# Optimization experiments

Measured on AMD Instinct MI355X. Metric: run time of the kernel, lower is better.

## Reference

```python
import jax, jax.numpy as jnp
import numpy as np

B, S, D, H = 4, 1024, 1024, 16
HD = D // H  # 64
NEG = -10000000.0


def setup_inputs() -> dict:
    key = jax.random.key(0)
    ks = jax.random.split(key, 8)
    x = jax.random.normal(ks[0], (B, S, D), dtype=jnp.float32)
    adj = jax.random.randint(ks[1], (B, S, S), 0, 2).astype(jnp.float32)
    scale = 1.0 / np.sqrt(D)
    Wq = jax.random.normal(ks[2], (D, D), dtype=jnp.float32) * scale
    bq = jnp.zeros((D,), dtype=jnp.float32)
    Wk = jax.random.normal(ks[3], (D, D), dtype=jnp.float32) * scale
    bk = jnp.zeros((D,), dtype=jnp.float32)
    Wv = jax.random.normal(ks[4], (D, D), dtype=jnp.float32) * scale
    bv = jnp.zeros((D,), dtype=jnp.float32)
    return {"x": x, "adj": adj, "Wq": Wq, "bq": bq, "Wk": Wk, "bk": bk, "Wv": Wv, "bv": bv}


def reference(x, adj, Wq, bq, Wk, bk, Wv, bv):
    # QKV projections, split into heads: [B,S,D] -> [B,H,S,HD]
    def heads(t):
        return t.reshape(B, S, H, HD).transpose(0, 2, 1, 3)

    q = heads(x @ Wq + bq)
    k = heads(x @ Wk + bk)
    v = heads(x @ Wv + bv)

    # scaled scores [B,H,S,S]
    scores = jnp.einsum('bhqd,bhkd->bhqk', q, k) / jnp.sqrt(jnp.asarray(HD, x.dtype))
    # adjacency mask: 0 where adj>=0.5 else -1e7, broadcast over heads
    mask_add = jnp.where(adj < 0.5, jnp.asarray(NEG, x.dtype), jnp.asarray(0.0, x.dtype))
    scores = scores + mask_add[:, None, :, :]

    probs = jax.nn.softmax(scores, axis=-1)
    ctx = jnp.einsum('bhqk,bhkd->bhqd', probs, v)  # [B,H,S,HD]
    ctx = ctx.transpose(0, 2, 1, 3).reshape(B, S, D)
    h = jax.nn.relu(ctx)
    return (h, adj)
```

## Files before the change

kernel.cpp:

```cpp
#include <hip/hip_runtime.h>

constexpr int Bn  = 4;
constexpr int Sn  = 1024;
constexpr int Dn  = 1024;
constexpr int Hn  = 16;
constexpr int HDn = 64;

using short8   = __attribute__((ext_vector_type(8))) short;
using float4v  = __attribute__((ext_vector_type(4))) float;
using float16v = __attribute__((ext_vector_type(16))) float;

__device__ __forceinline__ ushort f2bf(float f) {
    union { float f; unsigned u; } v; v.f = f;
    unsigned r = v.u + 0x7fff + ((v.u >> 16) & 1);
    return (ushort)(r >> 16);
}

__device__ __forceinline__ void gload16(const void* g, void* l) {
    __builtin_amdgcn_global_load_lds(
        (const __attribute__((address_space(1))) void*)g,
        (__attribute__((address_space(3))) void*)l, 16, 0, 0);
}

__global__ __launch_bounds__(256) void prep(
    const float* __restrict__ x,
    const float* __restrict__ Wq, const float* __restrict__ Wk,
    const float* __restrict__ Wv, const float* __restrict__ adj,
    ushort* __restrict__ xb, ushort* __restrict__ Wt, uint* __restrict__ Mb)
{
    const int bx  = blockIdx.x;
    const int tid = threadIdx.x;
    __shared__ __align__(16) ushort T[64 * 72];

    if (bx < 2048) {
        const size_t i = ((size_t)bx * 256 + tid) * 8;
        float4 a = *(const float4*)&x[i];
        float4 b = *(const float4*)&x[i + 4];
        ushort o[8] = {f2bf(a.x), f2bf(a.y), f2bf(a.z), f2bf(a.w),
                       f2bf(b.x), f2bf(b.y), f2bf(b.z), f2bf(b.w)};
        *(uint4*)&xb[i] = *(const uint4*)o;
    } else if (bx < 2816) {
        const int idx = bx - 2048;
        const int which = idx >> 8, rem = idx & 255;
        const float* __restrict__ W = (which == 0) ? Wq : (which == 1) ? Wk : Wv;
        ushort* __restrict__ O = Wt + (size_t)which * Dn * Dn;
        const int k0 = (rem & 15) * 64, n0 = (rem >> 4) * 64;

        const int kl = tid >> 4, nl = (tid & 15) * 4;
#pragma unroll
        for (int p = 0; p < 4; ++p) {
            float4 w4 = *(const float4*)&W[(size_t)(k0 + p * 16 + kl) * Dn + n0 + nl];
            T[(nl + 0) * 72 + p * 16 + kl] = f2bf(w4.x);
            T[(nl + 1) * 72 + p * 16 + kl] = f2bf(w4.y);
            T[(nl + 2) * 72 + p * 16 + kl] = f2bf(w4.z);
            T[(nl + 3) * 72 + p * 16 + kl] = f2bf(w4.w);
        }
        __syncthreads();
        const int nr = tid >> 2, kc = (tid & 3) * 16;
        uint4 u0 = *(const uint4*)&T[nr * 72 + kc];
        uint4 u1 = *(const uint4*)&T[nr * 72 + kc + 8];
        *(uint4*)&O[(size_t)(n0 + nr) * Dn + k0 + kc]     = u0;
        *(uint4*)&O[(size_t)(n0 + nr) * Dn + k0 + kc + 8] = u1;
    } else {
        const int rid  = (bx - 2816) * 256 + tid;
        const int lane = rid & 63;
        const int w    = (rid >> 6) & 3;
        const int kt   = (rid >> 8) & 15;
        const int qt   = (rid >> 12) & 7;
        const int b    = rid >> 15;
        const int col  = lane & 31, hi = lane >> 5;
        const int q    = qt * 128 + w * 32 + col;
        const float* arow = adj + ((size_t)b * Sn + q) * Sn + kt * 64;

        uint words[16];
#pragma unroll
        for (int mt = 0; mt < 2; ++mt)
#pragma unroll
            for (int pr = 0; pr < 8; ++pr) {
                const int r0 = 2 * pr;
                const int k0l = mt * 32 + (r0 & 3) + 8 * (r0 >> 2) + 4 * hi;
                float2 a = *(const float2*)&arow[k0l];
                words[mt * 8 + pr] = (a.x >= 0.5f ? 0x0000FFFFu : 0u) |
                                     (a.y >= 0.5f ? 0xFFFF0000u : 0u);
            }
        uint* dst = Mb + (size_t)rid * 16;
#pragma unroll
        for (int c = 0; c < 4; ++c)
            *(uint4*)&dst[c * 4] = make_uint4(words[c*4], words[c*4+1], words[c*4+2], words[c*4+3]);
    }
}

__global__ __launch_bounds__(256) void qkv_gemm(
    const ushort* __restrict__ xb, const ushort* __restrict__ Wt,
    const float* __restrict__ bq, const float* __restrict__ bk,
    const float* __restrict__ bv,
    ushort* __restrict__ Qb, ushort* __restrict__ Kb, ushort* __restrict__ Vb)
{
    const int which = blockIdx.z;
    const ushort* __restrict__ Bw   = Wt + (size_t)which * Dn * Dn;
    const float* __restrict__  bias = (which == 0) ? bq : (which == 1) ? bk : bv;
    ushort* __restrict__       Out  = (which == 0) ? Qb : (which == 1) ? Kb : Vb;
    const float scale = (which == 0) ? 0.18033688011112042f : 1.0f;

    const int n0   = blockIdx.x * 128;
    const int m0   = blockIdx.y * 128;
    const int tid  = threadIdx.x;
    const int wave = tid >> 6;
    const int lane = tid & 63;
    const int wm   = wave >> 1;
    const int wn   = wave & 1;

    __shared__ __align__(16) ushort As[128 * 32];
    __shared__ __align__(16) ushort Bs[128 * 32];

    const int L0 = wave * 64 + lane;
    const int r0s = L0 >> 2, c0s = (L0 & 3) * 8;
    const int L1 = L0 + 256;
    const int r1s = L1 >> 2, c1s = (L1 & 3) * 8;

    const ushort* pA0 = &xb[(size_t)(m0 + r0s) * Dn + c0s];
    const ushort* pA1 = &xb[(size_t)(m0 + r1s) * Dn + c1s];
    const ushort* pB0 = &Bw[(size_t)(n0 + r0s) * Dn + c0s];
    const ushort* pB1 = &Bw[(size_t)(n0 + r1s) * Dn + c1s];

    char* ldsA0 = (char*)As + wave * 1024;
    char* ldsA1 = (char*)As + wave * 1024 + 4096;
    char* ldsB0 = (char*)Bs + wave * 1024;
    char* ldsB1 = (char*)Bs + wave * 1024 + 4096;

    const int mlane = lane & 15;
    const int kg    = (lane >> 4) * 8;

    float4v acc[4][4];
    const float4v z4 = {0.f, 0.f, 0.f, 0.f};
#pragma unroll
    for (int i = 0; i < 4; ++i)
#pragma unroll
        for (int j = 0; j < 4; ++j) acc[i][j] = z4;

    for (int k0 = 0; k0 < Dn; k0 += 32) {
        __syncthreads();
        gload16(pA0, ldsA0);
        gload16(pA1, ldsA1);
        gload16(pB0, ldsB0);
        gload16(pB1, ldsB1);
        pA0 += 32; pA1 += 32; pB0 += 32; pB1 += 32;
        __syncthreads();

        short8 af[4], bf[4];
#pragma unroll
        for (int i = 0; i < 4; ++i)
            af[i] = *(const short8*)&As[(wm * 64 + i * 16 + mlane) * 32 + kg];
#pragma unroll
        for (int j = 0; j < 4; ++j)
            bf[j] = *(const short8*)&Bs[(wn * 64 + j * 16 + mlane) * 32 + kg];
#pragma unroll
        for (int i = 0; i < 4; ++i)
#pragma unroll
            for (int j = 0; j < 4; ++j)
                acc[i][j] = __builtin_amdgcn_mfma_f32_16x16x32_bf16(af[i], bf[j], acc[i][j], 0, 0, 0);
    }

    const int rb  = (lane >> 4) * 4;
    const int col = lane & 15;
#pragma unroll
    for (int j = 0; j < 4; ++j) {
        const int n  = n0 + wn * 64 + j * 16 + col;
        const float bias_n = bias[n];
        const int h  = n >> 6;
        const int hd = n & 63;
#pragma unroll
        for (int i = 0; i < 4; ++i) {
#pragma unroll
            for (int r = 0; r < 4; ++r) {
                const int m = m0 + wm * 64 + i * 16 + rb + r;
                const int b = m >> 10;
                const int s = m & 1023;
                size_t addr;
                if (which == 2)
                    addr = (((size_t)(b * Hn + h)) * HDn + hd) * Sn + s;
                else
                    addr = (((size_t)(b * Hn + h)) * Sn + s) * HDn + hd;
                Out[addr] = f2bf((acc[i][j][r] + bias_n) * scale);
            }
        }
    }
}

__global__ __launch_bounds__(256, 2) void attn_mfma(
    const ushort* __restrict__ Q, const ushort* __restrict__ K,
    const ushort* __restrict__ Vt, const uint* __restrict__ Mw,
    float* __restrict__ out)
{
    const int qt = blockIdx.x, h = blockIdx.y, b = blockIdx.z;
    const int tid  = threadIdx.x;
    const int w    = tid >> 6, lane = tid & 63;
    const int col  = lane & 31, hi = lane >> 5;

    const size_t hb = ((size_t)(b * Hn + h)) * Sn * HDn;
    const ushort* Kg = K + hb;
    const ushort* Vg = Vt + hb;

    __shared__ __align__(16) ushort Ks[2][64 * 72];
    __shared__ __align__(16) ushort Vs[2][64 * 72];

    short8 qf[4];
#pragma unroll
    for (int kp = 0; kp < 4; ++kp)
        qf[kp] = *(const short8*)&Q[hb +
            (size_t)(qt * 128 + w * 32 + col) * HDn + kp * 16 + hi * 8];

    float16v o_[2];
#pragma unroll
    for (int dt = 0; dt < 2; ++dt)
#pragma unroll
        for (int r = 0; r < 16; ++r) o_[dt][r] = 0.f;
    float ls = 0.f;

    const int c0 = tid, c1 = tid + 256;
    const int la0 = (c0 >> 3) * 72 + (c0 & 7) * 8;
    const int la1 = (c1 >> 3) * 72 + (c1 & 7) * 8;

    uint4 k0 = *(const uint4*)&Kg[(size_t)(c0 >> 3) * HDn + (c0 & 7) * 8];
    uint4 k1 = *(const uint4*)&Kg[(size_t)(c1 >> 3) * HDn + (c1 & 7) * 8];
    uint4 v0 = *(const uint4*)&Vg[(size_t)(c0 >> 3) * Sn + (c0 & 7) * 8];
    uint4 v1 = *(const uint4*)&Vg[(size_t)(c1 >> 3) * Sn + (c1 & 7) * 8];
    *(uint4*)&Ks[0][la0] = k0;  *(uint4*)&Ks[0][la1] = k1;
    *(uint4*)&Vs[0][la0] = v0;  *(uint4*)&Vs[0][la1] = v1;
    __syncthreads();

    const uint* mbase = Mw + ((size_t)((b * 8 + qt) * 16) * 4 + w) * 1024 + lane * 16;

    for (int kt = 0; kt < 16; ++kt) {
        const int cur = kt & 1;
        if (kt < 15) {
            k0 = *(const uint4*)&Kg[(size_t)((kt + 1) * 64 + (c0 >> 3)) * HDn + (c0 & 7) * 8];
            k1 = *(const uint4*)&Kg[(size_t)((kt + 1) * 64 + (c1 >> 3)) * HDn + (c1 & 7) * 8];
            v0 = *(const uint4*)&Vg[(size_t)(c0 >> 3) * Sn + (kt + 1) * 64 + (c0 & 7) * 8];
            v1 = *(const uint4*)&Vg[(size_t)(c1 >> 3) * Sn + (kt + 1) * 64 + (c1 & 7) * 8];
        }
        const uint* mp = mbase + (size_t)kt * 4096;
        uint4 mk4[4];
        mk4[0] = *(const uint4*)(mp);
        mk4[1] = *(const uint4*)(mp + 4);
        mk4[2] = *(const uint4*)(mp + 8);
        mk4[3] = *(const uint4*)(mp + 12);
        const uint* mka = (const uint*)mk4;

#pragma unroll
        for (int mt = 0; mt < 2; ++mt) {
            float16v s_;
#pragma unroll
            for (int r = 0; r < 16; ++r) s_[r] = 0.f;
#pragma unroll
            for (int kp = 0; kp < 4; ++kp) {
                short8 ak = *(const short8*)&Ks[cur][(mt * 32 + col) * 72 + kp * 16 + hi * 8];
                s_ = __builtin_amdgcn_mfma_f32_32x32x16_bf16(ak, qf[kp], s_, 0, 0, 0);
            }

            unsigned up[8];
#pragma unroll
            for (int pr = 0; pr < 8; ++pr) {
                const unsigned e0 = __float_as_uint(exp2f(s_[2 * pr]))     + 0x8000u;
                const unsigned e1 = __float_as_uint(exp2f(s_[2 * pr + 1])) + 0x8000u;
                const unsigned u  = __builtin_amdgcn_perm(e1, e0, 0x07060302u) & mka[mt * 8 + pr];
                up[pr] = u;
                ls += __uint_as_float(u << 16) + __uint_as_float(u & 0xffff0000u);
            }

#pragma unroll
            for (int kh = 0; kh < 2; ++kh) {
                const unsigned a0 = up[kh * 4 + 0], a1 = up[kh * 4 + 1];
                const unsigned a2 = up[kh * 4 + 2], a3 = up[kh * 4 + 3];
                const unsigned t0 = (unsigned)__shfl_xor((int)(hi ? a0 : a2), 32, 64);
                const unsigned t1 = (unsigned)__shfl_xor((int)(hi ? a1 : a3), 32, 64);
                union { short8 s; unsigned u[4]; } f;
                f.u[0] = hi ? t0 : a0;
                f.u[1] = hi ? t1 : a1;
                f.u[2] = hi ? a2 : t0;
                f.u[3] = hi ? a3 : t1;
                const int kp = mt * 2 + kh;
#pragma unroll
                for (int dt = 0; dt < 2; ++dt) {
                    short8 av = *(const short8*)&Vs[cur][(dt * 32 + col) * 72 + kp * 16 + hi * 8];
                    o_[dt] = __builtin_amdgcn_mfma_f32_32x32x16_bf16(av, f.s, o_[dt], 0, 0, 0);
                }
            }
        }

        if (kt < 15) {
            const int nxt = cur ^ 1;
            *(uint4*)&Ks[nxt][la0] = k0;  *(uint4*)&Ks[nxt][la1] = k1;
            *(uint4*)&Vs[nxt][la0] = v0;  *(uint4*)&Vs[nxt][la1] = v1;
        }
        __syncthreads();
    }

    float l = ls + (float)__shfl_xor((float)ls, 32, 64);
    const float inv = 1.0f / l;
    const int q = qt * 128 + w * 32 + col;
    float* op = &out[((size_t)b * Sn + q) * Dn + h * 64];
#pragma unroll
    for (int dt = 0; dt < 2; ++dt)
#pragma unroll
        for (int rg = 0; rg < 4; ++rg) {
            const int d = dt * 32 + rg * 8 + hi * 4;
            float4 o4;
            o4.x = fmaxf(o_[dt][rg * 4 + 0] * inv, 0.0f);
            o4.y = fmaxf(o_[dt][rg * 4 + 1] * inv, 0.0f);
            o4.z = fmaxf(o_[dt][rg * 4 + 2] * inv, 0.0f);
            o4.w = fmaxf(o_[dt][rg * 4 + 3] * inv, 0.0f);
            *(float4*)&op[d] = o4;
        }
}

extern "C" void kernel_launch(void* const* d_in, const int* in_sizes, int n_in,
                              void* d_out, int out_size, void* d_ws, size_t ws_size,
                              hipStream_t stream)
{
    const float* x   = (const float*)d_in[0];
    const float* adj = (const float*)d_in[1];
    const float* Wq  = (const float*)d_in[2];
    const float* bq  = (const float*)d_in[3];
    const float* Wk  = (const float*)d_in[4];
    const float* bk  = (const float*)d_in[5];
    const float* Wv  = (const float*)d_in[6];
    const float* bv  = (const float*)d_in[7];
    float* out = (float*)d_out;

    ushort* xb = (ushort*)d_ws;
    ushort* Wt = xb + (size_t)Bn * Sn * Dn;
    ushort* Qb = Wt + (size_t)3 * Dn * Dn;
    ushort* Kb = Qb + (size_t)Bn * Hn * Sn * HDn;
    ushort* Vb = Kb + (size_t)Bn * Hn * Sn * HDn;
    uint*   Mb = (uint*)(Vb + (size_t)Bn * Hn * Sn * HDn);

    prep<<<dim3(3328), 256, 0, stream>>>(x, Wq, Wk, Wv, adj, xb, Wt, Mb);

    qkv_gemm<<<dim3(Dn / 128, (Bn * Sn) / 128, 3), 256, 0, stream>>>(
        xb, Wt, bq, bk, bv, Qb, Kb, Vb);

    attn_mfma<<<dim3(8, Hn, Bn), 256, 0, stream>>>(Qb, Kb, Vb, Mb, out);

    hipMemcpyAsync(out + (size_t)Bn * Sn * Dn, adj,
                   (size_t)Bn * Sn * Sn * sizeof(float),
                   hipMemcpyDeviceToDevice, stream);
}
```

Baseline: 191.0 us.

## Split attention key range across waves with LDS reduction; split prep kernel

The attention kernel now gives each block 32 queries and has its four waves each handle a quarter of the key range. K and V are read straight from global memory instead of being staged in double-buffered LDS, and the partial outputs and row sums are combined through an LDS reduction at the end. The grid grows fourfold and launch bounds rise to 4 blocks per CU, trading more K/V global traffic for more parallelism and occupancy. The prep kernel is also split into three separate launches, which adds launch overhead.

```diff
diff --git a/kernel.cpp b/kernel.cpp
--- a/kernel.cpp
+++ b/kernel.cpp
@@ -22,72 +22,78 @@
         (__attribute__((address_space(3))) void*)l, 16, 0, 0);
 }
 
-__global__ __launch_bounds__(256) void prep(
-    const float* __restrict__ x,
+__global__ __launch_bounds__(256) void convert_x(const float* __restrict__ x,
+                                                 ushort* __restrict__ xb)
+{
+    const size_t i = ((size_t)blockIdx.x * 256 + threadIdx.x) * 8;
+    float4 a = *(const float4*)&x[i];
+    float4 b = *(const float4*)&x[i + 4];
+    ushort o[8] = {f2bf(a.x), f2bf(a.y), f2bf(a.z), f2bf(a.w),
+                   f2bf(b.x), f2bf(b.y), f2bf(b.z), f2bf(b.w)};
+    *(uint4*)&xb[i] = *(const uint4*)o;
+}
+
+__global__ __launch_bounds__(256) void transpose_w(
     const float* __restrict__ Wq, const float* __restrict__ Wk,
-    const float* __restrict__ Wv, const float* __restrict__ adj,
-    ushort* __restrict__ xb, ushort* __restrict__ Wt, uint* __restrict__ Mb)
-{
-    const int bx  = blockIdx.x;
-    const int tid = threadIdx.x;
+    const float* __restrict__ Wv, ushort* __restrict__ Wt)
+{
+    const int which = blockIdx.z;
+    const float* __restrict__ W = (which == 0) ? Wq : (which == 1) ? Wk : Wv;
+    ushort* __restrict__ O = Wt + (size_t)which * Dn * Dn;
+
+    const int k0 = blockIdx.x * 64;
+    const int n0 = blockIdx.y * 64;
+    const int t  = threadIdx.x;
+
     __shared__ __align__(16) ushort T[64 * 72];
 
-    if (bx < 2048) {
-        const size_t i = ((size_t)bx * 256 + tid) * 8;
-        float4 a = *(const float4*)&x[i];
-        float4 b = *(const float4*)&x[i + 4];
-        ushort o[8] = {f2bf(a.x), f2bf(a.y), f2bf(a.z), f2bf(a.w),
-                       f2bf(b.x), f2bf(b.y), f2bf(b.z), f2bf(b.w)};
-        *(uint4*)&xb[i] = *(const uint4*)o;
-    } else if (bx < 2816) {
-        const int idx = bx - 2048;
-        const int which = idx >> 8, rem = idx & 255;
-        const float* __restrict__ W = (which == 0) ? Wq : (which == 1) ? Wk : Wv;
-        ushort* __restrict__ O = Wt + (size_t)which * Dn * Dn;
-        const int k0 = (rem & 15) * 64, n0 = (rem >> 4) * 64;
-
-        const int kl = tid >> 4, nl = (tid & 15) * 4;
-#pragma unroll
-        for (int p = 0; p < 4; ++p) {
-            float4 w4 = *(const float4*)&W[(size_t)(k0 + p * 16 + kl) * Dn + n0 + nl];
-            T[(nl + 0) * 72 + p * 16 + kl] = f2bf(w4.x);
-            T[(nl + 1) * 72 + p * 16 + kl] = f2bf(w4.y);
-            T[(nl + 2) * 72 + p * 16 + kl] = f2bf(w4.z);
-            T[(nl + 3) * 72 + p * 16 + kl] = f2bf(w4.w);
+    const int kl = t >> 4;
+    const int nl = (t & 15) * 4;
+#pragma unroll
+    for (int p = 0; p < 4; ++p) {
+        float4 w = *(const float4*)&W[(size_t)(k0 + p * 16 + kl) * Dn + n0 + nl];
+        T[(nl + 0) * 72 + p * 16 + kl] = f2bf(w.x);
+        T[(nl + 1) * 72 + p * 16 + kl] = f2bf(w.y);
+        T[(nl + 2) * 72 + p * 16 + kl] = f2bf(w.z);
+        T[(nl + 3) * 72 + p * 16 + kl] = f2bf(w.w);
+    }
+    __syncthreads();
+    const int nr = t >> 2;
+    const int kc = (t & 3) * 16;
+    uint4 u0 = *(const uint4*)&T[nr * 72 + kc];
+    uint4 u1 = *(const uint4*)&T[nr * 72 + kc + 8];
+    *(uint4*)&O[(size_t)(n0 + nr) * Dn + k0 + kc]     = u0;
+    *(uint4*)&O[(size_t)(n0 + nr) * Dn + k0 + kc + 8] = u1;
+}
+
+__global__ __launch_bounds__(256) void build_mask(const float* __restrict__ adj,
+                                                  uint* __restrict__ Mb)
+{
+    const int rid  = blockIdx.x * 256 + threadIdx.x;
+    const int lane = rid & 63;
+    const int w    = (rid >> 6) & 3;
+    const int kt   = (rid >> 8) & 15;
+    const int qt   = (rid >> 12) & 7;
+    const int b    = rid >> 15;
+    const int col  = lane & 31, hi = lane >> 5;
+    const int q    = qt * 128 + w * 32 + col;
+    const float* arow = adj + ((size_t)b * Sn + q) * Sn + kt * 64;
+
+    uint words[16];
+#pragma unroll
+    for (int mt = 0; mt < 2; ++mt)
+#pragma unroll
+        for (int pr = 0; pr < 8; ++pr) {
+            const int r0 = 2 * pr;
+            const int k0l = mt * 32 + (r0 & 3) + 8 * (r0 >> 2) + 4 * hi;
+            float2 a = *(const float2*)&arow[k0l];
+            words[mt * 8 + pr] = (a.x >= 0.5f ? 0x0000FFFFu : 0u) |
+                                 (a.y >= 0.5f ? 0xFFFF0000u : 0u);
         }
-        __syncthreads();
-        const int nr = tid >> 2, kc = (tid & 3) * 16;
-        uint4 u0 = *(const uint4*)&T[nr * 72 + kc];
-        uint4 u1 = *(const uint4*)&T[nr * 72 + kc + 8];
-        *(uint4*)&O[(size_t)(n0 + nr) * Dn + k0 + kc]     = u0;
-        *(uint4*)&O[(size_t)(n0 + nr) * Dn + k0 + kc + 8] = u1;
-    } else {
-        const int rid  = (bx - 2816) * 256 + tid;
-        const int lane = rid & 63;
-        const int w    = (rid >> 6) & 3;
-        const int kt   = (rid >> 8) & 15;
-        const int qt   = (rid >> 12) & 7;
-        const int b    = rid >> 15;
-        const int col  = lane & 31, hi = lane >> 5;
-        const int q    = qt * 128 + w * 32 + col;
-        const float* arow = adj + ((size_t)b * Sn + q) * Sn + kt * 64;
-
-        uint words[16];
-#pragma unroll
-        for (int mt = 0; mt < 2; ++mt)
-#pragma unroll
-            for (int pr = 0; pr < 8; ++pr) {
-                const int r0 = 2 * pr;
-                const int k0l = mt * 32 + (r0 & 3) + 8 * (r0 >> 2) + 4 * hi;
-                float2 a = *(const float2*)&arow[k0l];
-                words[mt * 8 + pr] = (a.x >= 0.5f ? 0x0000FFFFu : 0u) |
-                                     (a.y >= 0.5f ? 0xFFFF0000u : 0u);
-            }
-        uint* dst = Mb + (size_t)rid * 16;
-#pragma unroll
-        for (int c = 0; c < 4; ++c)
-            *(uint4*)&dst[c * 4] = make_uint4(words[c*4], words[c*4+1], words[c*4+2], words[c*4+3]);
-    }
+    uint* dst = Mb + (size_t)rid * 16;
+#pragma unroll
+    for (int c = 0; c < 4; ++c)
+        *(uint4*)&dst[c * 4] = make_uint4(words[c*4], words[c*4+1], words[c*4+2], words[c*4+3]);
 }
 
 __global__ __launch_bounds__(256) void qkv_gemm(
@@ -187,12 +193,12 @@
     }
 }
 
-__global__ __launch_bounds__(256, 2) void attn_mfma(
+__global__ __launch_bounds__(256, 4) void attn_mfma(
     const ushort* __restrict__ Q, const ushort* __restrict__ K,
     const ushort* __restrict__ Vt, const uint* __restrict__ Mw,
     float* __restrict__ out)
 {
-    const int qt = blockIdx.x, h = blockIdx.y, b = blockIdx.z;
+    const int qsub = blockIdx.x, h = blockIdx.y, b = blockIdx.z;
     const int tid  = threadIdx.x;
     const int w    = tid >> 6, lane = tid & 63;
     const int col  = lane & 31, hi = lane >> 5;
@@ -201,14 +207,12 @@
     const ushort* Kg = K + hb;
     const ushort* Vg = Vt + hb;
 
-    __shared__ __align__(16) ushort Ks[2][64 * 72];
-    __shared__ __align__(16) ushort Vs[2][64 * 72];
+    __shared__ __align__(16) float red[3 * 64 * 34];
 
     short8 qf[4];
 #pragma unroll
     for (int kp = 0; kp < 4; ++kp)
-        qf[kp] = *(const short8*)&Q[hb +
-            (size_t)(qt * 128 + w * 32 + col) * HDn + kp * 16 + hi * 8];
+        qf[kp] = *(const short8*)&Q[hb + (size_t)(qsub * 32 + col) * HDn + kp * 16 + hi * 8];
 
     float16v o_[2];
 #pragma unroll
@@ -217,61 +221,43 @@
         for (int r = 0; r < 16; ++r) o_[dt][r] = 0.f;
     float ls = 0.f;
 
-    const int c0 = tid, c1 = tid + 256;
-    const int la0 = (c0 >> 3) * 72 + (c0 & 7) * 8;
-    const int la1 = (c1 >> 3) * 72 + (c1 & 7) * 8;
-
-    uint4 k0 = *(const uint4*)&Kg[(size_t)(c0 >> 3) * HDn + (c0 & 7) * 8];
-    uint4 k1 = *(const uint4*)&Kg[(size_t)(c1 >> 3) * HDn + (c1 & 7) * 8];
-    uint4 v0 = *(const uint4*)&Vg[(size_t)(c0 >> 3) * Sn + (c0 & 7) * 8];
-    uint4 v1 = *(const uint4*)&Vg[(size_t)(c1 >> 3) * Sn + (c1 & 7) * 8];
-    *(uint4*)&Ks[0][la0] = k0;  *(uint4*)&Ks[0][la1] = k1;
-    *(uint4*)&Vs[0][la0] = v0;  *(uint4*)&Vs[0][la1] = v1;
-    __syncthreads();
-
-    const uint* mbase = Mw + ((size_t)((b * 8 + qt) * 16) * 4 + w) * 1024 + lane * 16;
-
-    for (int kt = 0; kt < 16; ++kt) {
-        const int cur = kt & 1;
-        if (kt < 15) {
-            k0 = *(const uint4*)&Kg[(size_t)((kt + 1) * 64 + (c0 >> 3)) * HDn + (c0 & 7) * 8];
-            k1 = *(const uint4*)&Kg[(size_t)((kt + 1) * 64 + (c1 >> 3)) * HDn + (c1 & 7) * 8];
-            v0 = *(const uint4*)&Vg[(size_t)(c0 >> 3) * Sn + (kt + 1) * 64 + (c0 & 7) * 8];
-            v1 = *(const uint4*)&Vg[(size_t)(c1 >> 3) * Sn + (kt + 1) * 64 + (c1 & 7) * 8];
-        }
-        const uint* mp = mbase + (size_t)kt * 4096;
-        uint4 mk4[4];
-        mk4[0] = *(const uint4*)(mp);
-        mk4[1] = *(const uint4*)(mp + 4);
-        mk4[2] = *(const uint4*)(mp + 8);
-        mk4[3] = *(const uint4*)(mp + 12);
-        const uint* mka = (const uint*)mk4;
+    const int qt = qsub >> 2, wq = qsub & 3;
+    const uint* mb0 = Mw + ((size_t)((b * 8 + qt) * 16) * 4 + wq) * 1024 + lane * 16;
+
+#pragma unroll
+    for (int kk = 0; kk < 4; ++kk) {
+        const int kt = w * 4 + kk;
+        const uint* mp = mb0 + (size_t)kt * 4096;
 
 #pragma unroll
         for (int mt = 0; mt < 2; ++mt) {
             float16v s_;
 #pragma unroll
             for (int r = 0; r < 16; ++r) s_[r] = 0.f;
+            const ushort* krow = &Kg[(size_t)(kt * 64 + mt * 32 + col) * HDn + hi * 8];
 #pragma unroll
             for (int kp = 0; kp < 4; ++kp) {
-                short8 ak = *(const short8*)&Ks[cur][(mt * 32 + col) * 72 + kp * 16 + hi * 8];
+                short8 ak = *(const short8*)&krow[kp * 16];
                 s_ = __builtin_amdgcn_mfma_f32_32x32x16_bf16(ak, qf[kp], s_, 0, 0, 0);
             }
 
+            uint4 mA = *(const uint4*)(mp + mt * 8);
+            uint4 mB = *(const uint4*)(mp + mt * 8 + 4);
+            const uint mka[8] = {mA.x, mA.y, mA.z, mA.w, mB.x, mB.y, mB.z, mB.w};
             unsigned up[8];
 #pragma unroll
             for (int pr = 0; pr < 8; ++pr) {
                 const unsigned e0 = __float_as_uint(exp2f(s_[2 * pr]))     + 0x8000u;
                 const unsigned e1 = __float_as_uint(exp2f(s_[2 * pr + 1])) + 0x8000u;
-                const unsigned u  = __builtin_amdgcn_perm(e1, e0, 0x07060302u) & mka[mt * 8 + pr];
+                const unsigned u  = __builtin_amdgcn_perm(e1, e0, 0x07060302u) & mka[pr];
                 up[pr] = u;
                 ls += __uint_as_float(u << 16) + __uint_as_float(u & 0xffff0000u);
             }
 
 #pragma unroll
-            for (int kh = 0; kh < 2; ++kh) {
-                const unsigned a0 = up[kh * 4 + 0], a1 = up[kh * 4 + 1];
-                const unsigned a2 = up[kh * 4 + 2], a3 = up[kh * 4 + 3];
+            for (int kkh = 0; kkh < 2; ++kkh) {
+                const unsigned a0 = up[kkh * 4 + 0], a1 = up[kkh * 4 + 1];
+                const unsigned a2 = up[kkh * 4 + 2], a3 = up[kkh * 4 + 3];
                 const unsigned t0 = (unsigned)__shfl_xor((int)(hi ? a0 : a2), 32, 64);
                 const unsigned t1 = (unsigned)__shfl_xor((int)(hi ? a1 : a3), 32, 64);
                 union { short8 s; unsigned u[4]; } f;
@@ -279,39 +265,57 @@
                 f.u[1] = hi ? t1 : a1;
                 f.u[2] = hi ? a2 : t0;
                 f.u[3] = hi ? a3 : t1;
-                const int kp = mt * 2 + kh;
+                const int kp = mt * 2 + kkh;
 #pragma unroll
                 for (int dt = 0; dt < 2; ++dt) {
-                    short8 av = *(const short8*)&Vs[cur][(dt * 32 + col) * 72 + kp * 16 + hi * 8];
+                    short8 av = *(const short8*)&Vg[(size_t)(dt * 32 + col) * Sn
+                                                    + kt * 64 + kp * 16 + hi * 8];
                     o_[dt] = __builtin_amdgcn_mfma_f32_32x32x16_bf16(av, f.s, o_[dt], 0, 0, 0);
                 }
             }
         }
-
-        if (kt < 15) {
-            const int nxt = cur ^ 1;
-            *(uint4*)&Ks[nxt][la0] = k0;  *(uint4*)&Ks[nxt][la1] = k1;
-            *(uint4*)&Vs[nxt][la0] = v0;  *(uint4*)&Vs[nxt][la1] = v1;
+    }
+
+    if (w > 0) {
+        float* p = red + (size_t)((w - 1) * 64 + lane) * 34;
+#pragma unroll
+        for (int dt = 0; dt < 2; ++dt)
+#pragma unroll
+            for (int c = 0; c < 4; ++c)
+                *(float4*)&p[dt * 16 + c * 4] = make_float4(
+                    o_[dt][c * 4 + 0], o_[dt][c * 4 + 1],
+                    o_[dt][c * 4 + 2], o_[dt][c * 4 + 3]);
+        p[32] = ls;
+    }
+    __syncthreads();
+    if (w == 0) {
+#pragma unroll
+        for (int ww = 0; ww < 3; ++ww) {
+            const float* p = red + (size_t)(ww * 64 + lane) * 34;
+#pragma unroll
+            for (int dt = 0; dt < 2; ++dt)
+#pragma unroll
+                for (int r = 0; r < 16; ++r) o_[dt][r] += p[dt * 16 + r];
+            ls += p[32];
         }
-        __syncthreads();
-    }
-
-    float l = ls + (float)__shfl_xor((float)ls, 32, 64);
-    const float inv = 1.0f / l;
-    const int q = qt * 128 + w * 32 + col;
-    float* op = &out[((size_t)b * Sn + q) * Dn + h * 64];
-#pragma unroll
-    for (int dt = 0; dt < 2; ++dt)
-#pragma unroll
-        for (int rg = 0; rg < 4; ++rg) {
-            const int d = dt * 32 + rg * 8 + hi * 4;
-            float4 o4;
-            o4.x = fmaxf(o_[dt][rg * 4 + 0] * inv, 0.0f);
-            o4.y = fmaxf(o_[dt][rg * 4 + 1] * inv, 0.0f);
-            o4.z = fmaxf(o_[dt][rg * 4 + 2] * inv, 0.0f);
-            o4.w = fmaxf(o_[dt][rg * 4 + 3] * inv, 0.0f);
-            *(float4*)&op[d] = o4;
-        }
+
+        float l = ls + (float)__shfl_xor((float)ls, 32, 64);
+        const float inv = 1.0f / l;
+        const int q = qsub * 32 + col;
+        float* op = &out[((size_t)b * Sn + q) * Dn + h * 64];
+#pragma unroll
+        for (int dt = 0; dt < 2; ++dt)
+#pragma unroll
+            for (int rg = 0; rg < 4; ++rg) {
+                const int d = dt * 32 + rg * 8 + hi * 4;
+                float4 o4;
+                o4.x = fmaxf(o_[dt][rg * 4 + 0] * inv, 0.0f);
+                o4.y = fmaxf(o_[dt][rg * 4 + 1] * inv, 0.0f);
+                o4.z = fmaxf(o_[dt][rg * 4 + 2] * inv, 0.0f);
+                o4.w = fmaxf(o_[dt][rg * 4 + 3] * inv, 0.0f);
+                *(float4*)&op[d] = o4;
+            }
+    }
 }
 
 extern "C" void kernel_launch(void* const* d_in, const int* in_sizes, int n_in,
@@ -335,12 +339,14 @@
     ushort* Vb = Kb + (size_t)Bn * Hn * Sn * HDn;
     uint*   Mb = (uint*)(Vb + (size_t)Bn * Hn * Sn * HDn);
 
-    prep<<<dim3(3328), 256, 0, stream>>>(x, Wq, Wk, Wv, adj, xb, Wt, Mb);
+    convert_x<<<dim3(2048), 256, 0, stream>>>(x, xb);
+    transpose_w<<<dim3(16, 16, 3), 256, 0, stream>>>(Wq, Wk, Wv, Wt);
+    build_mask<<<dim3(512), 256, 0, stream>>>(adj, Mb);
 
     qkv_gemm<<<dim3(Dn / 128, (Bn * Sn) / 128, 3), 256, 0, stream>>>(
         xb, Wt, bq, bk, bv, Qb, Kb, Vb);
 
-    attn_mfma<<<dim3(8, Hn, Bn), 256, 0, stream>>>(Qb, Kb, Vb, Mb, out);
+    attn_mfma<<<dim3(32, Hn, Bn), 256, 0, stream>>>(Qb, Kb, Vb, Mb, out);
 
     hipMemcpyAsync(out + (size_t)Bn * Sn * Dn, adj,
                    (size_t)Bn * Sn * Sn * sizeof(float),
```

New measurement: 227.8 us. 1.19x slower.

## Fuse adj copy into mask build and stage GEMM epilogue through LDS

Applied to the files above, without the earlier changes.

The adjacency pass-through copy moves out of a separate device memcpy and into the mask-building kernel. That kernel now reads adj once with coalesced float4 loads, writes the copy, and packs mask words from an LDS tile. The QKV GEMM epilogue now stages bf16 results in shared memory and writes them with coalesced 16-byte stores, replacing the scattered 2-byte stores, which were especially bad for the transposed V layout. The prep kernel is split into three separate launches, which adds launch overhead and makes the GEMM's LDS footprint larger.

```diff
diff --git a/kernel.cpp b/kernel.cpp
--- a/kernel.cpp
+++ b/kernel.cpp
@@ -22,55 +22,79 @@
         (__attribute__((address_space(3))) void*)l, 16, 0, 0);
 }
 
-__global__ __launch_bounds__(256) void prep(
-    const float* __restrict__ x,
+__global__ __launch_bounds__(256) void convert_x(const float* __restrict__ x,
+                                                 ushort* __restrict__ xb)
+{
+    const size_t i = ((size_t)blockIdx.x * 256 + threadIdx.x) * 8;
+    float4 a = *(const float4*)&x[i];
+    float4 b = *(const float4*)&x[i + 4];
+    ushort o[8] = {f2bf(a.x), f2bf(a.y), f2bf(a.z), f2bf(a.w),
+                   f2bf(b.x), f2bf(b.y), f2bf(b.z), f2bf(b.w)};
+    *(uint4*)&xb[i] = *(const uint4*)o;
+}
+
+__global__ __launch_bounds__(256) void transpose_w(
     const float* __restrict__ Wq, const float* __restrict__ Wk,
-    const float* __restrict__ Wv, const float* __restrict__ adj,
-    ushort* __restrict__ xb, ushort* __restrict__ Wt, uint* __restrict__ Mb)
-{
-    const int bx  = blockIdx.x;
+    const float* __restrict__ Wv, ushort* __restrict__ Wt)
+{
+    const int which = blockIdx.z;
+    const float* __restrict__ W = (which == 0) ? Wq : (which == 1) ? Wk : Wv;
+    ushort* __restrict__ O = Wt + (size_t)which * Dn * Dn;
+
+    const int k0 = blockIdx.x * 64;
+    const int n0 = blockIdx.y * 64;
+    const int t  = threadIdx.x;
+
+    __shared__ __align__(16) ushort T[64 * 72];
+
+    const int kl = t >> 4;
+    const int nl = (t & 15) * 4;
+#pragma unroll
+    for (int p = 0; p < 4; ++p) {
+        float4 w = *(const float4*)&W[(size_t)(k0 + p * 16 + kl) * Dn + n0 + nl];
+        T[(nl + 0) * 72 + p * 16 + kl] = f2bf(w.x);
+        T[(nl + 1) * 72 + p * 16 + kl] = f2bf(w.y);
+        T[(nl + 2) * 72 + p * 16 + kl] = f2bf(w.z);
+        T[(nl + 3) * 72 + p * 16 + kl] = f2bf(w.w);
+    }
+    __syncthreads();
+    const int nr = t >> 2;
+    const int kc = (t & 3) * 16;
+    uint4 u0 = *(const uint4*)&T[nr * 72 + kc];
+    uint4 u1 = *(const uint4*)&T[nr * 72 + kc + 8];
+    *(uint4*)&O[(size_t)(n0 + nr) * Dn + k0 + kc]     = u0;
+    *(uint4*)&O[(size_t)(n0 + nr) * Dn + k0 + kc + 8] = u1;
+}
+
+__global__ __launch_bounds__(256) void build_mask_copy(
+    const float* __restrict__ adj, uint* __restrict__ Mb,
+    float* __restrict__ out)
+{
+    const int qt = blockIdx.x, ktp = blockIdx.y, b = blockIdx.z;
     const int tid = threadIdx.x;
-    __shared__ __align__(16) ushort T[64 * 72];
-
-    if (bx < 2048) {
-        const size_t i = ((size_t)bx * 256 + tid) * 8;
-        float4 a = *(const float4*)&x[i];
-        float4 b = *(const float4*)&x[i + 4];
-        ushort o[8] = {f2bf(a.x), f2bf(a.y), f2bf(a.z), f2bf(a.w),
-                       f2bf(b.x), f2bf(b.y), f2bf(b.z), f2bf(b.w)};
-        *(uint4*)&xb[i] = *(const uint4*)o;
-    } else if (bx < 2816) {
-        const int idx = bx - 2048;
-        const int which = idx >> 8, rem = idx & 255;
-        const float* __restrict__ W = (which == 0) ? Wq : (which == 1) ? Wk : Wv;
-        ushort* __restrict__ O = Wt + (size_t)which * Dn * Dn;
-        const int k0 = (rem & 15) * 64, n0 = (rem >> 4) * 64;
-
-        const int kl = tid >> 4, nl = (tid & 15) * 4;
-#pragma unroll
-        for (int p = 0; p < 4; ++p) {
-            float4 w4 = *(const float4*)&W[(size_t)(k0 + p * 16 + kl) * Dn + n0 + nl];
-            T[(nl + 0) * 72 + p * 16 + kl] = f2bf(w4.x);
-            T[(nl + 1) * 72 + p * 16 + kl] = f2bf(w4.y);
-            T[(nl + 2) * 72 + p * 16 + kl] = f2bf(w4.z);
-            T[(nl + 3) * 72 + p * 16 + kl] = f2bf(w4.w);
-        }
-        __syncthreads();
-        const int nr = tid >> 2, kc = (tid & 3) * 16;
-        uint4 u0 = *(const uint4*)&T[nr * 72 + kc];
-        uint4 u1 = *(const uint4*)&T[nr * 72 + kc + 8];
-        *(uint4*)&O[(size_t)(n0 + nr) * Dn + k0 + kc]     = u0;
-        *(uint4*)&O[(size_t)(n0 + nr) * Dn + k0 + kc + 8] = u1;
-    } else {
-        const int rid  = (bx - 2816) * 256 + tid;
-        const int lane = rid & 63;
-        const int w    = (rid >> 6) & 3;
-        const int kt   = (rid >> 8) & 15;
-        const int qt   = (rid >> 12) & 7;
-        const int b    = rid >> 15;
-        const int col  = lane & 31, hi = lane >> 5;
-        const int q    = qt * 128 + w * 32 + col;
-        const float* arow = adj + ((size_t)b * Sn + q) * Sn + kt * 64;
+    __shared__ char msk[128][68];
+
+    const int lane = tid & 63, w = tid >> 6;
+    const int col = lane & 31, hi = lane >> 5;
+
+    float* ocopy = out + (size_t)Bn * Sn * Dn;
+
+#pragma unroll
+    for (int kk = 0; kk < 2; ++kk) {
+        const int kt = ktp * 2 + kk;
+
+        const int r16 = tid >> 4, c4 = (tid & 15) * 4;
+#pragma unroll
+        for (int p = 0; p < 8; ++p) {
+            const int row = p * 16 + r16;
+            const size_t gi = ((size_t)b * Sn + qt * 128 + row) * Sn + kt * 64 + c4;
+            float4 a = *(const float4*)&adj[gi];
+            *(float4*)&ocopy[gi] = a;
+            char* mr = &msk[row][c4];
+            mr[0] = a.x >= 0.5f; mr[1] = a.y >= 0.5f;
+            mr[2] = a.z >= 0.5f; mr[3] = a.w >= 0.5f;
+        }
+        __syncthreads();
 
         uint words[16];
 #pragma unroll
@@ -78,15 +102,16 @@
 #pragma unroll
             for (int pr = 0; pr < 8; ++pr) {
                 const int r0 = 2 * pr;
-                const int k0l = mt * 32 + (r0 & 3) + 8 * (r0 >> 2) + 4 * hi;
-                float2 a = *(const float2*)&arow[k0l];
-                words[mt * 8 + pr] = (a.x >= 0.5f ? 0x0000FFFFu : 0u) |
-                                     (a.y >= 0.5f ? 0xFFFF0000u : 0u);
-            }
-        uint* dst = Mb + (size_t)rid * 16;
+                const int kl = mt * 32 + (r0 & 3) + 8 * (r0 >> 2) + 4 * hi;
+                words[mt * 8 + pr] = (msk[w * 32 + col][kl]     ? 0x0000FFFFu : 0u) |
+                                     (msk[w * 32 + col][kl + 1] ? 0xFFFF0000u : 0u);
+            }
+        uint* dst = Mb + ((((size_t)(b * 8 + qt) * 16 + kt) * 4 + w) * 64 + lane) * 16;
 #pragma unroll
         for (int c = 0; c < 4; ++c)
-            *(uint4*)&dst[c * 4] = make_uint4(words[c*4], words[c*4+1], words[c*4+2], words[c*4+3]);
+            *(uint4*)&dst[c * 4] =
+                make_uint4(words[c*4], words[c*4+1], words[c*4+2], words[c*4+3]);
+        __syncthreads();
     }
 }
 
@@ -110,8 +135,9 @@
     const int wm   = wave >> 1;
     const int wn   = wave & 1;
 
-    __shared__ __align__(16) ushort As[128 * 32];
-    __shared__ __align__(16) ushort Bs[128 * 32];
+    __shared__ __align__(16) ushort pool[128 * 136];
+    ushort* As = pool;
+    ushort* Bs = pool + 128 * 32;
 
     const int L0 = wave * 64 + lane;
     const int r0s = L0 >> 2, c0s = (L0 & 3) * 8;
@@ -161,29 +187,53 @@
                 acc[i][j] = __builtin_amdgcn_mfma_f32_16x16x32_bf16(af[i], bf[j], acc[i][j], 0, 0, 0);
     }
 
-    const int rb  = (lane >> 4) * 4;
-    const int col = lane & 15;
-#pragma unroll
-    for (int j = 0; j < 4; ++j) {
-        const int n  = n0 + wn * 64 + j * 16 + col;
-        const float bias_n = bias[n];
-        const int h  = n >> 6;
-        const int hd = n & 63;
-#pragma unroll
-        for (int i = 0; i < 4; ++i) {
-#pragma unroll
-            for (int r = 0; r < 4; ++r) {
-                const int m = m0 + wm * 64 + i * 16 + rb + r;
-                const int b = m >> 10;
-                const int s = m & 1023;
-                size_t addr;
-                if (which == 2)
-                    addr = (((size_t)(b * Hn + h)) * HDn + hd) * Sn + s;
-                else
-                    addr = (((size_t)(b * Hn + h)) * Sn + s) * HDn + hd;
-                Out[addr] = f2bf((acc[i][j][r] + bias_n) * scale);
-            }
-        }
+    const int rb    = (lane >> 4) * 4;
+    const int col16 = lane & 15;
+    const int bb    = m0 >> 10;
+    const int s0    = m0 & 1023;
+    ushort* C2 = pool;
+
+    __syncthreads();
+    if (which == 2) {
+#pragma unroll
+        for (int j = 0; j < 4; ++j) {
+            const int nl = wn * 64 + j * 16 + col16;
+            const float bias_n = bias[n0 + nl];
+#pragma unroll
+            for (int i = 0; i < 4; ++i) {
+                ushort h4[4];
+#pragma unroll
+                for (int r = 0; r < 4; ++r) h4[r] = f2bf(acc[i][j][r] + bias_n);
+                *(uint2*)&C2[nl * 136 + wm * 64 + i * 16 + rb] = *(const uint2*)h4;
+            }
+        }
+        __syncthreads();
+        const int n  = tid >> 1, mh = (tid & 1) * 64;
+        const int gn = n0 + n, hh = gn >> 6, hd = gn & 63;
+        ushort* dst = &Out[(((size_t)(bb * Hn + hh)) * HDn + hd) * Sn + s0 + mh];
+#pragma unroll
+        for (int c = 0; c < 8; ++c)
+            *(uint4*)&dst[c * 8] = *(const uint4*)&C2[n * 136 + mh + c * 8];
+    } else {
+#pragma unroll
+        for (int j = 0; j < 4; ++j) {
+            const int nl = wn * 64 + j * 16 + col16;
+            const float bias_n = bias[n0 + nl];
+#pragma unroll
+            for (int i = 0; i < 4; ++i)
+#pragma unroll
+                for (int r = 0; r < 4; ++r)
+                    C2[(wm * 64 + i * 16 + rb + r) * 136 + nl] =
+                        f2bf((acc[i][j][r] + bias_n) * scale);
+        }
+        __syncthreads();
+        const int m  = tid >> 1, nh = (tid & 1) * 64;
+        const int gn = n0 + nh, hh = gn >> 6;
+        const int s  = s0 + m;
+        ushort* dst = &Out[(((size_t)(bb * Hn + hh)) * Sn + s) * HDn];
+#pragma unroll
+        for (int c = 0; c < 8; ++c)
+            *(uint4*)&dst[c * 8] = *(const uint4*)&C2[m * 136 + nh + c * 8];
     }
 }
 
@@ -335,14 +385,12 @@
     ushort* Vb = Kb + (size_t)Bn * Hn * Sn * HDn;
     uint*   Mb = (uint*)(Vb + (size_t)Bn * Hn * Sn * HDn);
 
-    prep<<<dim3(3328), 256, 0, stream>>>(x, Wq, Wk, Wv, adj, xb, Wt, Mb);
+    convert_x<<<dim3(2048), 256, 0, stream>>>(x, xb);
+    transpose_w<<<dim3(16, 16, 3), 256, 0, stream>>>(Wq, Wk, Wv, Wt);
+    build_mask_copy<<<dim3(8, 8, 4), 256, 0, stream>>>(adj, Mb, out);
 
     qkv_gemm<<<dim3(Dn / 128, (Bn * Sn) / 128, 3), 256, 0, stream>>>(
         xb, Wt, bq, bk, bv, Qb, Kb, Vb);
 
     attn_mfma<<<dim3(8, Hn, Bn), 256, 0, stream>>>(Qb, Kb, Vb, Mb, out);
-
-    hipMemcpyAsync(out + (size_t)Bn * Sn * Dn, adj,
-                   (size_t)Bn * Sn * Sn * sizeof(float),
-                   hipMemcpyDeviceToDevice, stream);
-}
+}
```

New measurement: 200.0 us. 1.05x slower.

## Fuse adj passthrough copy into mask prep kernel with coalesced LDS staging

Applied to the files above, without the earlier changes.

Removes the separate device-to-device memcpy of adj into the output and does that copy inside the prep kernel's mask blocks, which already read adj. The mask blocks now load a 128x64 adj tile with coalesced float4 reads, write it straight to the output, and stage boolean mask bytes in shared memory before packing the MFMA-layout mask words. This saves one full 16MB read of adj and one extra launch. In exchange, prep takes on more write traffic and an extra barrier.

```diff
diff --git a/kernel.cpp b/kernel.cpp
--- a/kernel.cpp
+++ b/kernel.cpp
@@ -26,11 +26,12 @@
     const float* __restrict__ x,
     const float* __restrict__ Wq, const float* __restrict__ Wk,
     const float* __restrict__ Wv, const float* __restrict__ adj,
-    ushort* __restrict__ xb, ushort* __restrict__ Wt, uint* __restrict__ Mb)
+    ushort* __restrict__ xb, ushort* __restrict__ Wt, uint* __restrict__ Mb,
+    float* __restrict__ out)
 {
     const int bx  = blockIdx.x;
     const int tid = threadIdx.x;
-    __shared__ __align__(16) ushort T[64 * 72];
+    __shared__ __align__(16) ushort pool[64 * 72];
 
     if (bx < 2048) {
         const size_t i = ((size_t)bx * 256 + tid) * 8;
@@ -45,6 +46,7 @@
         const float* __restrict__ W = (which == 0) ? Wq : (which == 1) ? Wk : Wv;
         ushort* __restrict__ O = Wt + (size_t)which * Dn * Dn;
         const int k0 = (rem & 15) * 64, n0 = (rem >> 4) * 64;
+        ushort* T = pool;
 
         const int kl = tid >> 4, nl = (tid & 15) * 4;
 #pragma unroll
@@ -62,31 +64,42 @@
         *(uint4*)&O[(size_t)(n0 + nr) * Dn + k0 + kc]     = u0;
         *(uint4*)&O[(size_t)(n0 + nr) * Dn + k0 + kc + 8] = u1;
     } else {
-        const int rid  = (bx - 2816) * 256 + tid;
-        const int lane = rid & 63;
-        const int w    = (rid >> 6) & 3;
-        const int kt   = (rid >> 8) & 15;
-        const int qt   = (rid >> 12) & 7;
-        const int b    = rid >> 15;
-        const int col  = lane & 31, hi = lane >> 5;
-        const int q    = qt * 128 + w * 32 + col;
-        const float* arow = adj + ((size_t)b * Sn + q) * Sn + kt * 64;
-
+        const int idx = bx - 2816;
+        const int kt = idx & 15, qt = (idx >> 4) & 7, b = idx >> 7;
+        char* msk = (char*)pool;
+
+        float* ocopy = out + (size_t)Bn * Sn * Dn;
+        const int r16 = tid >> 4, c4 = (tid & 15) * 4;
+#pragma unroll
+        for (int p = 0; p < 8; ++p) {
+            const int row = p * 16 + r16;
+            const size_t gi = ((size_t)b * Sn + qt * 128 + row) * Sn + kt * 64 + c4;
+            float4 a = *(const float4*)&adj[gi];
+            *(float4*)&ocopy[gi] = a;
+            char* mr = &msk[row * 68 + c4];
+            mr[0] = a.x >= 0.5f; mr[1] = a.y >= 0.5f;
+            mr[2] = a.z >= 0.5f; mr[3] = a.w >= 0.5f;
+        }
+        __syncthreads();
+
+        const int lane = tid & 63, w = tid >> 6;
+        const int col = lane & 31, hi = lane >> 5;
         uint words[16];
 #pragma unroll
         for (int mt = 0; mt < 2; ++mt)
 #pragma unroll
             for (int pr = 0; pr < 8; ++pr) {
                 const int r0 = 2 * pr;
-                const int k0l = mt * 32 + (r0 & 3) + 8 * (r0 >> 2) + 4 * hi;
-                float2 a = *(const float2*)&arow[k0l];
-                words[mt * 8 + pr] = (a.x >= 0.5f ? 0x0000FFFFu : 0u) |
-                                     (a.y >= 0.5f ? 0xFFFF0000u : 0u);
-            }
-        uint* dst = Mb + (size_t)rid * 16;
+                const int kl = mt * 32 + (r0 & 3) + 8 * (r0 >> 2) + 4 * hi;
+                const char* mr = &msk[(w * 32 + col) * 68];
+                words[mt * 8 + pr] = (mr[kl]     ? 0x0000FFFFu : 0u) |
+                                     (mr[kl + 1] ? 0xFFFF0000u : 0u);
+            }
+        uint* dst = Mb + ((((size_t)(b * 8 + qt) * 16 + kt) * 4 + w) * 64 + lane) * 16;
 #pragma unroll
         for (int c = 0; c < 4; ++c)
-            *(uint4*)&dst[c * 4] = make_uint4(words[c*4], words[c*4+1], words[c*4+2], words[c*4+3]);
+            *(uint4*)&dst[c * 4] =
+                make_uint4(words[c*4], words[c*4+1], words[c*4+2], words[c*4+3]);
     }
 }
 
@@ -335,14 +348,10 @@
     ushort* Vb = Kb + (size_t)Bn * Hn * Sn * HDn;
     uint*   Mb = (uint*)(Vb + (size_t)Bn * Hn * Sn * HDn);
 
-    prep<<<dim3(3328), 256, 0, stream>>>(x, Wq, Wk, Wv, adj, xb, Wt, Mb);
+    prep<<<dim3(3328), 256, 0, stream>>>(x, Wq, Wk, Wv, adj, xb, Wt, Mb, out);
 
     qkv_gemm<<<dim3(Dn / 128, (Bn * Sn) / 128, 3), 256, 0, stream>>>(
         xb, Wt, bq, bk, bv, Qb, Kb, Vb);
 
     attn_mfma<<<dim3(8, Hn, Bn), 256, 0, stream>>>(Qb, Kb, Vb, Mb, out);
-
-    hipMemcpyAsync(out + (size_t)Bn * Sn * Dn, adj,
-                   (size_t)Bn * Sn * Sn * sizeof(float),
-                   hipMemcpyDeviceToDevice, stream);
-}
+}
```

After: 188.0 us. No clear change (-1.6%).
